# Optimization experiments

Hardware: AMD Instinct MI355X
Metric: run time of the kernel (lower is better)

## Reference

```python
import jax, jax.numpy as jnp
import numpy as np

E = 8  # path_num


def setup_inputs() -> dict:
    key = jax.random.key(0)
    k1, k2, k3 = jax.random.split(key, 3)
    N, D = 8192, 1024
    x = jax.random.normal(k1, (N, D), dtype=jnp.float32)
    hot_mask = jax.random.randint(k2, (N, E), 0, 2, dtype=jnp.int32)  # multi-hot 0/1
    score = jax.random.uniform(k3, (N, E), dtype=jnp.float32)
    return {"x": x, "hot_mask": hot_mask, "score": score}


def reference(x, hot_mask, score):
    # MoE dispatch (route_logic='1d', transform=True):
    # for each expert e, gather tokens n with hot_mask[n, e] == 1 in order,
    # scaled by score[n, e]. Outputs padded to capacity N (zeros beyond count).
    N, D = x.shape
    mask = hot_mask > 0                                   # [N, E]
    ranks = jnp.cumsum(hot_mask, axis=0) - 1              # [N, E] position within expert
    dest = jnp.where(mask, ranks, N)                      # dropped tokens -> dump slot N
    tags = jnp.arange(N, dtype=jnp.int64)                 # flow_tag (arange via pack_invalid_flow)
    scale = score * mask.astype(score.dtype)              # [N, E]

    def per_expert(dest_e, scale_e, mask_e):
        vals = x * scale_e[:, None]                       # [N, D] scaled (zero if not routed)
        out = jnp.zeros((N + 1, D), x.dtype).at[dest_e].add(vals)[:N]
        tag_out = jnp.zeros((N + 1,), jnp.int64).at[dest_e].add(
            jnp.where(mask_e, tags, 0))[:N]               # gathered out_flow_tag, 0-padded
        return out, tag_out

    out_data, out_tags = jax.vmap(per_expert, in_axes=(1, 1, 1))(dest, scale, mask)
    counts = jnp.sum(hot_mask, axis=0)                    # [E] tokens per expert
    return out_data, out_tags, counts
```

## Files before the change

### kernel.cpp

```cpp
#include <hip/hip_runtime.h>

#define N_TOK 8192
#define D_DIM 1024
#define E_NUM 8
#define D4 (D_DIM / 4)

__global__ __launch_bounds__(256) void dispatch_scan_kernel(
    const int* __restrict__ hot_mask,
    int* __restrict__ src,
    float* __restrict__ out_tags,
    float* __restrict__ out_counts)
{
    const int e = blockIdx.x;
    const int t = threadIdx.x;
    constexpr int TPT = N_TOK / 256;

    __shared__ int lds[256];

    const int base = t * TPT;
    int m[TPT];
    int tot = 0;
    #pragma unroll
    for (int i = 0; i < TPT; ++i) {
        m[i] = hot_mask[(size_t)(base + i) * E_NUM + e];
        tot += m[i];
    }

    lds[t] = tot;
    __syncthreads();

    for (int off = 1; off < 256; off <<= 1) {
        int other = (t >= off) ? lds[t - off] : 0;
        __syncthreads();
        if (t >= off) lds[t] += other;
        __syncthreads();
    }

    const int incl  = lds[t];
    const int excl  = incl - tot;
    const int count = lds[255];

    int r = excl;
    #pragma unroll
    for (int i = 0; i < TPT; ++i) {
        if (m[i]) {
            const int n = base + i;
            src[(size_t)e * N_TOK + r]      = n;
            out_tags[(size_t)e * N_TOK + r] = (float)n;
            ++r;
        }
    }

    for (int rr = count + t; rr < N_TOK; rr += 256) {
        src[(size_t)e * N_TOK + rr]      = -1;
        out_tags[(size_t)e * N_TOK + rr] = 0.0f;
    }

    if (t == 0) out_counts[e] = (float)count;
}

__global__ __launch_bounds__(256) void dispatch_gather_kernel(
    const float4* __restrict__ x,
    const float* __restrict__ score,
    const int* __restrict__ src,
    float4* __restrict__ out)
{
    const int row = blockIdx.x;
    const int e   = row >> 13;
    const int c   = threadIdx.x;

    const int n = src[row];

    float4 v;
    if (n >= 0) {
        const float s = score[(size_t)n * E_NUM + e];
        const float4 xv = x[(size_t)n * D4 + c];
        v.x = xv.x * s;
        v.y = xv.y * s;
        v.z = xv.z * s;
        v.w = xv.w * s;
    } else {
        v.x = 0.0f; v.y = 0.0f; v.z = 0.0f; v.w = 0.0f;
    }

    out[(size_t)row * D4 + c] = v;
}

extern "C" void kernel_launch(void* const* d_in, const int* in_sizes, int n_in,
                              void* d_out, int out_size, void* d_ws, size_t ws_size,
                              hipStream_t stream) {
    const float* x        = (const float*)d_in[0];
    const int*   hot_mask = (const int*)d_in[1];
    const float* score    = (const float*)d_in[2];

    float* out        = (float*)d_out;
    float* out_data   = out;
    float* out_tags   = out + (size_t)E_NUM * N_TOK * D_DIM;
    float* out_counts = out_tags + (size_t)E_NUM * N_TOK;

    int* src = (int*)d_ws;

    dispatch_scan_kernel<<<E_NUM, 256, 0, stream>>>(hot_mask, src, out_tags, out_counts);
    dispatch_gather_kernel<<<E_NUM * N_TOK, 256, 0, stream>>>(
        (const float4*)x, score, src, (float4*)out_data);
}
```

Before: 68.50 us.

## Switch gather to token-major scatter to read each input row once

The scan now records each token's destination rank per expert instead of a per-slot source index. The data kernel launches one block per token: it loads the row once and writes scaled copies to every routed expert slot. Separate blocks zero the padded slots past each expert's count. This cuts redundant reads of x, but adds more blocks and scattered row writes.

```diff
diff --git a/kernel.cpp b/kernel.cpp
--- a/kernel.cpp
+++ b/kernel.cpp
@@ -5,9 +5,11 @@
 #define E_NUM 8
 #define D4 (D_DIM / 4)
 
+
 __global__ __launch_bounds__(256) void dispatch_scan_kernel(
     const int* __restrict__ hot_mask,
-    int* __restrict__ src,
+    int* __restrict__ dest,
+    int* __restrict__ counts_i,
     float* __restrict__ out_tags,
     float* __restrict__ out_counts)
 {
@@ -43,47 +45,62 @@
     int r = excl;
     #pragma unroll
     for (int i = 0; i < TPT; ++i) {
+        const int n = base + i;
         if (m[i]) {
-            const int n = base + i;
-            src[(size_t)e * N_TOK + r]      = n;
+            dest[(size_t)n * E_NUM + e]     = r;
             out_tags[(size_t)e * N_TOK + r] = (float)n;
             ++r;
+        } else {
+            dest[(size_t)n * E_NUM + e] = -1;
         }
     }
 
     for (int rr = count + t; rr < N_TOK; rr += 256) {
-        src[(size_t)e * N_TOK + rr]      = -1;
         out_tags[(size_t)e * N_TOK + rr] = 0.0f;
     }
 
-    if (t == 0) out_counts[e] = (float)count;
+    if (t == 0) {
+        counts_i[e]   = count;
+        out_counts[e] = (float)count;
+    }
 }
 
-__global__ __launch_bounds__(256) void dispatch_gather_kernel(
+__global__ __launch_bounds__(256) void dispatch_scatter_kernel(
     const float4* __restrict__ x,
     const float* __restrict__ score,
-    const int* __restrict__ src,
+    const int* __restrict__ dest,
+    const int* __restrict__ counts_i,
     float4* __restrict__ out)
 {
-    const int row = blockIdx.x;
-    const int e   = row >> 13;
-    const int c   = threadIdx.x;
+    const int b = blockIdx.x;
+    const int c = threadIdx.x;
 
-    const int n = src[row];
-
-    float4 v;
-    if (n >= 0) {
-        const float s = score[(size_t)n * E_NUM + e];
+    if (b < N_TOK) {
+        const int n = b;
         const float4 xv = x[(size_t)n * D4 + c];
-        v.x = xv.x * s;
-        v.y = xv.y * s;
-        v.z = xv.z * s;
-        v.w = xv.w * s;
+        #pragma unroll
+        for (int e = 0; e < E_NUM; ++e) {
+            const int r = dest[(size_t)n * E_NUM + e];
+            if (r >= 0) {
+                const float s = score[(size_t)n * E_NUM + e];
+                float4 v;
+                v.x = xv.x * s;
+                v.y = xv.y * s;
+                v.z = xv.z * s;
+                v.w = xv.w * s;
+                out[((size_t)e * N_TOK + r) * D4 + c] = v;
+            }
+        }
     } else {
-        v.x = 0.0f; v.y = 0.0f; v.z = 0.0f; v.w = 0.0f;
+        const int row = b - N_TOK;
+        const int e   = row >> 13;
+        const int r   = row & (N_TOK - 1);
+        if (r >= counts_i[e]) {
+            float4 z;
+            z.x = 0.0f; z.y = 0.0f; z.z = 0.0f; z.w = 0.0f;
+            out[(size_t)row * D4 + c] = z;
+        }
     }
-
-    out[(size_t)row * D4 + c] = v;
 }
 
 extern "C" void kernel_launch(void* const* d_in, const int* in_sizes, int n_in,
@@ -98,9 +115,12 @@
     float* out_tags   = out + (size_t)E_NUM * N_TOK * D_DIM;
     float* out_counts = out_tags + (size_t)E_NUM * N_TOK;
 
-    int* src = (int*)d_ws;
+    int* dest     = (int*)d_ws;
+    int* counts_i = dest + (size_t)N_TOK * E_NUM;
 
-    dispatch_scan_kernel<<<E_NUM, 256, 0, stream>>>(hot_mask, src, out_tags, out_counts);
-    dispatch_gather_kernel<<<E_NUM * N_TOK, 256, 0, stream>>>(
-        (const float4*)x, score, src, (float4*)out_data);
+    dispatch_scan_kernel<<<E_NUM, 256, 0, stream>>>(
+        hot_mask, dest, counts_i, out_tags, out_counts);
+
+    dispatch_scatter_kernel<<<N_TOK + E_NUM * N_TOK, 256, 0, stream>>>(
+        (const float4*)x, score, dest, counts_i, (float4*)out_data);
 }
```

New measurement: 63.03 us. -8.0%, faster.
